# Kernel tuning notes

Hardware: AMD Instinct MI355X
Metric: run time of the kernel (lower is better)

Reference implementation:

```python
import jax, jax.numpy as jnp
import numpy as np

N = 100000   # nodes
E = 1600000  # edges
G = 512      # graphs
IN_F = 128
HID = 64
EPS = 1e-5


def setup_inputs() -> dict:
    key = jax.random.key(0)
    ks = jax.random.split(key, 16)
    x = jax.random.normal(ks[0], (N, IN_F), dtype=jnp.float32)
    edge_index = jax.random.randint(ks[1], (2, E), 0, N, dtype=jnp.int64)
    batch = jnp.sort(jax.random.randint(ks[2], (N,), 0, G, dtype=jnp.int64))
    s = 0.05
    return {
        'x': x, 'edge_index': edge_index, 'batch': batch,
        'W1': jax.random.normal(ks[3], (IN_F, HID), jnp.float32) * s,
        'b1': jax.random.normal(ks[4], (HID,), jnp.float32) * s,
        'g1': jax.random.uniform(ks[5], (HID,), jnp.float32),
        'be1': jax.random.normal(ks[6], (HID,), jnp.float32) * s,
        'rm1': jnp.zeros((HID,), jnp.float32),
        'rv1': jnp.ones((HID,), jnp.float32),
        'W2': jax.random.normal(ks[7], (HID, HID), jnp.float32) * s,
        'b2': jax.random.normal(ks[8], (HID,), jnp.float32) * s,
        'g2': jax.random.uniform(ks[9], (HID,), jnp.float32),
        'be2': jax.random.normal(ks[10], (HID,), jnp.float32) * s,
        'rm2': jnp.zeros((HID,), jnp.float32),
        'rv2': jnp.ones((HID,), jnp.float32),
        'Wh1': jax.random.normal(ks[11], (2 * HID, HID), jnp.float32) * s,
        'bh1': jax.random.normal(ks[12], (HID,), jnp.float32) * s,
        'Wh2': jax.random.normal(ks[13], (HID, HID // 2), jnp.float32) * s,
        'bh2': jnp.zeros((HID // 2,), jnp.float32),
        'Wh3': jax.random.normal(ks[14], (HID // 2, 1), jnp.float32) * s,
        'bh3': jnp.zeros((1,), jnp.float32),
    }


def _gcn(h, W, b, src, dst):
    # GCNConv with added self-loops and symmetric D^{-1/2} A D^{-1/2} normalization
    hw = h @ W                                   # [N, HID]
    deg = jnp.ones((N,), hw.dtype).at[dst].add(1.0)  # in-degree + self-loop
    dinv = jax.lax.rsqrt(deg)
    norm = dinv[src] * dinv[dst]                 # [E]
    agg = jax.ops.segment_sum(hw[src] * norm[:, None], dst, num_segments=N)
    return agg + hw * (dinv * dinv)[:, None] + b  # self-loop term + bias


def _bn(x, g, b, rm, rv):
    return (x - rm) * jax.lax.rsqrt(rv + EPS) * g + b


def reference(x, edge_index, batch, W1, b1, g1, be1, rm1, rv1,
              W2, b2, g2, be2, rm2, rv2, Wh1, bh1, Wh2, bh2, Wh3, bh3):
    src, dst = edge_index[0], edge_index[1]
    # layer 0 (no residual: dim change 128 -> 64)
    h = jax.nn.relu(_bn(_gcn(x, W1, b1, src, dst), g1, be1, rm1, rv1))
    # layer 1 with residual
    h = h + jax.nn.relu(_bn(_gcn(h, W2, b2, src, dst), g2, be2, rm2, rv2))
    # global mean + max pooling per graph
    ones = jnp.ones((N,), h.dtype)
    cnt = jnp.maximum(jax.ops.segment_sum(ones, batch, num_segments=G), 1.0)
    h_mean = jax.ops.segment_sum(h, batch, num_segments=G) / cnt[:, None]
    h_max = jax.ops.segment_max(h, batch, num_segments=G)
    hg = jnp.concatenate([h_mean, h_max], axis=-1)   # [G, 2*HID]
    # MLP head (dropout disabled in eval)
    z = jax.nn.relu(hg @ Wh1 + bh1)
    z = jax.nn.relu(z @ Wh2 + bh2)
    out = z @ Wh3 + bh3
    return jax.nn.sigmoid(out).squeeze(-1)           # [G]
```

## Files before the change

kernel.cpp:

```cpp
#include <hip/hip_runtime.h>
#include <math.h>

#define NN 100000
#define EE 1600000
#define GG 512
#define INF_ 128
#define HID 64
#define EPS 1e-5f

#define NBUK 391
#define P1_TILES 98
#define SETUP_B 25
#define POOL_WORDS (GG * 64 * 2 + GG)
#define ZERO_B ((POOL_WORDS + 255) / 256)

typedef unsigned int uint32;
typedef __attribute__((ext_vector_type(8))) short bf16x8;
typedef __attribute__((ext_vector_type(4))) float f32x4;

static __device__ inline uint32 f2bf(float f) {
    uint32 u = __float_as_uint(f);
    return (u + 0x7FFFu + ((u >> 16) & 1u)) >> 16;
}
static __device__ inline float bf_lo(uint32 u) { return __uint_as_float(u << 16); }
static __device__ inline float bf_hi(uint32 u) { return __uint_as_float(u & 0xFFFF0000u); }


__global__ __launch_bounds__(256) void k_hist1(const int* __restrict__ ei,
        int* __restrict__ hblk,
        const float* b1, const float* g1, const float* be1,
        const float* rm1, const float* rv1,
        const float* b2, const float* g2, const float* be2,
        const float* rm2, const float* rv2, float* sc,
        const float* W1, uint32* Wt1b, const float* W2, uint32* Wt2b,
        float* poolz) {
    int b = blockIdx.x, t = threadIdx.x;
    if (b < P1_TILES) {
        __shared__ int h[NBUK];
        for (int i = t; i < NBUK; i += 256) h[i] = 0;
        __syncthreads();
        const int4* dst4 = (const int4*)(ei + EE);
        int base4 = b * 4096;
        for (int j = 0; j < 16; ++j) {
            int i4 = base4 + j * 256 + t;
            if (i4 < EE / 4) {
                int4 d = dst4[i4];
                atomicAdd(&h[d.x >> 8], 1);
                atomicAdd(&h[d.y >> 8], 1);
                atomicAdd(&h[d.z >> 8], 1);
                atomicAdd(&h[d.w >> 8], 1);
            }
        }
        __syncthreads();
        for (int i = t; i < NBUK; i += 256) hblk[b * NBUK + i] = h[i];
    } else if (b < P1_TILES + SETUP_B) {
        int i = (b - P1_TILES) * 256 + t;
        if (i < 4096) {
            int n = i >> 6, kp = (i & 63) * 2;
            Wt1b[i] = f2bf(W1[(size_t)kp * 64 + n]) |
                      (f2bf(W1[(size_t)(kp + 1) * 64 + n]) << 16);
        } else if (i < 6144) {
            int j = i - 4096;
            int n = j >> 5, kp = (j & 31) * 2;
            Wt2b[j] = f2bf(W2[(size_t)kp * 64 + n]) |
                      (f2bf(W2[(size_t)(kp + 1) * 64 + n]) << 16);
        } else if (i < 6208) {
            int l = i - 6144;
            float s1 = g1[l] * rsqrtf(rv1[l] + EPS);
            sc[l]       = s1;
            sc[64 + l]  = (b1[l] - rm1[l]) * s1 + be1[l];
            float s2 = g2[l] * rsqrtf(rv2[l] + EPS);
            sc[128 + l] = s2;
            sc[192 + l] = (b2[l] - rm2[l]) * s2 + be2[l];
        }
    } else {
        int i = (b - P1_TILES - SETUP_B) * 256 + t;
        if (i < POOL_WORDS) poolz[i] = 0.f;
    }
}

__global__ void k_scan2(const int* __restrict__ hblk, int* __restrict__ bbase,
                        int* __restrict__ rbase, int* __restrict__ offs,
                        uint32* __restrict__ hwb) {
    __shared__ int wsum[8];
    int t = threadIdx.x;
    int lane = t & 63, w = t >> 6;
    if (t < 32) hwb[(size_t)NN * 32 + t] = 0u;
    int c = 0;
    if (t < NBUK)
        for (int b = 0; b < P1_TILES; ++b) c += hblk[b * NBUK + t];
    int v = c;
    for (int d = 1; d < 64; d <<= 1) { int n = __shfl_up(v, d); if (lane >= d) v += n; }
    if (lane == 63) wsum[w] = v;
    __syncthreads();
    int pre = 0;
    for (int q = 0; q < w; ++q) pre += wsum[q];
    int excl = pre + v - c;
    if (t <= NBUK) bbase[t] = excl;
    if (t == 0) offs[NN] = EE;
    if (t < NBUK) {
        int run = excl;
        for (int b = 0; b < P1_TILES; ++b) {
            rbase[b * NBUK + t] = run;
            run += hblk[b * NBUK + t];
        }
    }
}

__global__ __launch_bounds__(256) void k_p1b(const int* __restrict__ ei,
                                             const int* __restrict__ rbase,
                                             uint32* __restrict__ pairs) {
    __shared__ int h[NBUK];
    int b = blockIdx.x, t = threadIdx.x;
    for (int i = t; i < NBUK; i += 256) h[i] = rbase[b * NBUK + i];
    __syncthreads();
    const int4* src4 = (const int4*)ei;
    const int4* dst4 = (const int4*)(ei + EE);
    int base4 = b * 4096;
    for (int j = 0; j < 16; ++j) {
        int i4 = base4 + j * 256 + t;
        if (i4 < EE / 4) {
            int4 d = dst4[i4];
            int4 s = src4[i4];
            int p0 = atomicAdd(&h[d.x >> 8], 1);
            pairs[p0] = ((uint32)s.x << 8) | (uint32)(d.x & 255);
            int p1 = atomicAdd(&h[d.y >> 8], 1);
            pairs[p1] = ((uint32)s.y << 8) | (uint32)(d.y & 255);
            int p2 = atomicAdd(&h[d.z >> 8], 1);
            pairs[p2] = ((uint32)s.z << 8) | (uint32)(d.z & 255);
            int p3 = atomicAdd(&h[d.w >> 8], 1);
            pairs[p3] = ((uint32)s.w << 8) | (uint32)(d.w & 255);
        }
    }
}

__global__ __launch_bounds__(256) void k_p2(const uint32* __restrict__ pairs,
                                            const int* __restrict__ bbase,
                                            int* __restrict__ offs, float* __restrict__ dinv,
                                            int* __restrict__ col) {
    int b = blockIdx.x, t = threadIdx.x;
    int nbase = b << 8;
    int ebase = bbase[b], eend = bbase[b + 1];
    int m = eend - ebase;
    __shared__ int cnt[256];
    __shared__ int wsum[4];
    cnt[t] = 0;
    __syncthreads();
    for (int i = t; i < m; i += 256)
        atomicAdd(&cnt[pairs[ebase + i] & 255u], 1);
    __syncthreads();
    int c = cnt[t];
    int lane = t & 63, w = t >> 6;
    int v = c;
    for (int d = 1; d < 64; d <<= 1) { int n = __shfl_up(v, d); if (lane >= d) v += n; }
    if (lane == 63) wsum[w] = v;
    __syncthreads();
    int pre = 0;
    for (int q = 0; q < w; ++q) pre += wsum[q];
    int excl = pre + v - c;
    int node = nbase + t;
    if (node < NN) {
        offs[node] = ebase + excl;
        dinv[node] = rsqrtf(1.f + (float)c);
    }
    __syncthreads();
    cnt[t] = excl;
    __syncthreads();
    for (int i = t; i < m; i += 256) {
        uint32 u = pairs[ebase + i];
        int loc = atomicAdd(&cnt[u & 255u], 1);
        col[ebase + loc] = (int)(u >> 8);
    }
}

template <int K>
__global__ __launch_bounds__(256) void k_gemm_mfma(const float* __restrict__ X,
                                                   const uint32* __restrict__ Wtb,
                                                   const float* __restrict__ dinv,
                                                   uint32* __restrict__ outb, int nrows) {
    constexpr int KP = K + 8;
    __shared__ alignas(16) unsigned short Al[64 * KP];
    __shared__ alignas(16) unsigned short Bl[64 * KP];
    int tid = threadIdx.x;
    for (int i = tid; i < 64 * (K / 2); i += 256) {
        int n = i / (K / 2), kp = i % (K / 2);
        *(uint32*)&Bl[n * KP + kp * 2] = Wtb[i];
    }
    int r0 = blockIdx.x * 64;
    const float* Xb = X + (size_t)r0 * K;
    int limit = (nrows - r0) * K;
    for (int f = tid * 4; f < 64 * K; f += 1024) {
        float4 v = {0.f, 0.f, 0.f, 0.f};
        if (f + 3 < limit) v = *(const float4*)&Xb[f];
        int row = f / K, kpos = f % K;
        ushort4 pk;
        pk.x = (unsigned short)f2bf(v.x);
        pk.y = (unsigned short)f2bf(v.y);
        pk.z = (unsigned short)f2bf(v.z);
        pk.w = (unsigned short)f2bf(v.w);
        *(ushort4*)&Al[row * KP + kpos] = pk;
    }
    __syncthreads();
    int lane = tid & 63, wv = tid >> 6;
    int m = lane & 15, quad = lane >> 4;
    f32x4 acc0 = {0.f, 0.f, 0.f, 0.f}, acc1 = acc0, acc2 = acc0, acc3 = acc0;
    int arow = wv * 16 + m;
#pragma unroll
    for (int k0 = 0; k0 < K; k0 += 32) {
        int koff = k0 + quad * 8;
        bf16x8 a = *(const bf16x8*)&Al[arow * KP + koff];
        bf16x8 b0 = *(const bf16x8*)&Bl[(0 * 16 + m) * KP + koff];
        bf16x8 b1 = *(const bf16x8*)&Bl[(1 * 16 + m) * KP + koff];
        bf16x8 b2 = *(const bf16x8*)&Bl[(2 * 16 + m) * KP + koff];
        bf16x8 b3 = *(const bf16x8*)&Bl[(3 * 16 + m) * KP + koff];
        acc0 = __builtin_amdgcn_mfma_f32_16x16x32_bf16(a, b0, acc0, 0, 0, 0);
        acc1 = __builtin_amdgcn_mfma_f32_16x16x32_bf16(a, b1, acc1, 0, 0, 0);
        acc2 = __builtin_amdgcn_mfma_f32_16x16x32_bf16(a, b2, acc2, 0, 0, 0);
        acc3 = __builtin_amdgcn_mfma_f32_16x16x32_bf16(a, b3, acc3, 0, 0, 0);
    }
    float dv[4];
#pragma unroll
    for (int reg = 0; reg < 4; ++reg) {
        int row = r0 + wv * 16 + quad * 4 + reg;
        dv[reg] = (row < nrows) ? dinv[row] : 0.f;
    }
    const float* accs[4] = {(const float*)&acc0, (const float*)&acc1,
                            (const float*)&acc2, (const float*)&acc3};
#pragma unroll
    for (int nt = 0; nt < 4; ++nt) {
#pragma unroll
        for (int reg = 0; reg < 4; ++reg) {
            float val = accs[nt][reg] * dv[reg];
            float nxt = __shfl_down(val, 1);
            int row = r0 + wv * 16 + quad * 4 + reg;
            if (((m & 1) == 0) && row < nrows)
                outb[(size_t)row * 32 + nt * 8 + (m >> 1)] =
                    f2bf(val) | (f2bf(nxt) << 16);
        }
    }
}

__global__ void k_gcn_gather(const uint32* __restrict__ hwb, const int* __restrict__ col,
                             const int* __restrict__ offs,
                             const float* __restrict__ dinv, const float* __restrict__ scale,
                             const float* __restrict__ shift, const float* __restrict__ resid,
                             float* __restrict__ out) {
    int node = blockIdx.x * 4 + (threadIdx.x >> 6);
    if (node >= NN) return;
    int lane = threadIdx.x & 63;
    int half = lane >> 5;
    int fl = lane & 31;
    int e0 = offs[node], e1 = offs[node + 1];
    float di = dinv[node];
    uint32 uself = hwb[(size_t)node * 32 + fl];
    float ax0 = 0.f, ay0 = 0.f, ax1 = 0.f, ay1 = 0.f;
    for (int base = e0; base < e1; base += 64) {
        int m = e1 - base; if (m > 64) m = 64;
        int srcv = NN;
        if (lane < m) srcv = col[base + lane];
        for (int j = 0; j < m; j += 16) {
            int s0 = __shfl(srcv, j + half);
            int s1 = __shfl(srcv, j + 2 + half);
            int s2 = __shfl(srcv, j + 4 + half);
            int s3 = __shfl(srcv, j + 6 + half);
            int s4 = __shfl(srcv, j + 8 + half);
            int s5 = __shfl(srcv, j + 10 + half);
            int s6 = __shfl(srcv, j + 12 + half);
            int s7 = __shfl(srcv, j + 14 + half);
            uint32 u0 = hwb[(size_t)s0 * 32 + fl];
            uint32 u1 = hwb[(size_t)s1 * 32 + fl];
            uint32 u2 = hwb[(size_t)s2 * 32 + fl];
            uint32 u3 = hwb[(size_t)s3 * 32 + fl];
            uint32 u4 = hwb[(size_t)s4 * 32 + fl];
            uint32 u5 = hwb[(size_t)s5 * 32 + fl];
            uint32 u6 = hwb[(size_t)s6 * 32 + fl];
            uint32 u7 = hwb[(size_t)s7 * 32 + fl];
            ax0 += bf_lo(u0); ay0 += bf_hi(u0);
            ax1 += bf_lo(u1); ay1 += bf_hi(u1);
            ax0 += bf_lo(u2); ay0 += bf_hi(u2);
            ax1 += bf_lo(u3); ay1 += bf_hi(u3);
            ax0 += bf_lo(u4); ay0 += bf_hi(u4);
            ax1 += bf_lo(u5); ay1 += bf_hi(u5);
            ax0 += bf_lo(u6); ay0 += bf_hi(u6);
            ax1 += bf_lo(u7); ay1 += bf_hi(u7);
        }
    }
    float ax = ax0 + ax1, ay = ay0 + ay1;
    ax += __shfl(ax, fl + 32);
    ay += __shfl(ay, fl + 32);
    if (half == 0) {
        float vx = fmaf((ax + bf_lo(uself)) * di, scale[2 * fl],     shift[2 * fl]);
        float vy = fmaf((ay + bf_hi(uself)) * di, scale[2 * fl + 1], shift[2 * fl + 1]);
        vx = fmaxf(vx, 0.f);
        vy = fmaxf(vy, 0.f);
        if (resid) {
            float2 rv = *(const float2*)&resid[(size_t)node * 64 + 2 * fl];
            vx += rv.x; vy += rv.y;
        }
        float2 o; o.x = vx; o.y = vy;
        *(float2*)&out[(size_t)node * 64 + 2 * fl] = o;
    }
}

__global__ __launch_bounds__(256) void k_pool(const float* __restrict__ h,
                       const int* __restrict__ batch,
                       float* __restrict__ msum, float* __restrict__ mmax,
                       float* __restrict__ gcnt) {
    int lane = threadIdx.x & 63;
    int wv = threadIdx.x >> 6;
    int i0 = blockIdx.x * 128 + wv * 32;
    if (i0 >= NN) return;
    int i1 = i0 + 32; if (i1 > NN) i1 = NN;
    int cur = batch[i0];
    float sum = 0.f, mx = 0.f; int c = 0;
    for (int i = i0; i < i1; ++i) {
        int g = batch[i];
        if (g != cur) {
            atomicAdd(&msum[cur * 64 + lane], sum);
            atomicMax((unsigned int*)&mmax[cur * 64 + lane], __float_as_uint(mx));
            if (lane == 0) atomicAdd(&gcnt[cur], (float)c);
            sum = 0.f; mx = 0.f; c = 0; cur = g;
        }
        float v = h[(long)i * 64 + lane];
        sum += v; mx = fmaxf(mx, v); ++c;
    }
    atomicAdd(&msum[cur * 64 + lane], sum);
    atomicMax((unsigned int*)&mmax[cur * 64 + lane], __float_as_uint(mx));
    if (lane == 0) atomicAdd(&gcnt[cur], (float)c);
}

__global__ void k_head(const float* __restrict__ msum, const float* __restrict__ mmax,
                       const float* __restrict__ gcnt,
                       const float* __restrict__ Wh1, const float* __restrict__ bh1,
                       const float* __restrict__ Wh2, const float* __restrict__ bh2,
                       const float* __restrict__ Wh3, const float* __restrict__ bh3,
                       float* __restrict__ out) {
    int g = blockIdx.x, t = threadIdx.x;
    __shared__ float hg[128];
    __shared__ float z1[64];
    __shared__ float z2[32];
    float c = fmaxf(gcnt[g], 1.f);
    hg[t]      = msum[g * 64 + t] / c;
    hg[64 + t] = mmax[g * 64 + t];
    __syncthreads();
    float acc = bh1[t];
#pragma unroll 8
    for (int k = 0; k < 128; ++k) acc = fmaf(hg[k], Wh1[k * 64 + t], acc);
    z1[t] = fmaxf(acc, 0.f);
    __syncthreads();
    if (t < 32) {
        float a2 = bh2[t];
#pragma unroll 8
        for (int k = 0; k < 64; ++k) a2 = fmaf(z1[k], Wh2[k * 32 + t], a2);
        z2[t] = fmaxf(a2, 0.f);
    }
    __syncthreads();
    if (t == 0) {
        float a3 = bh3[0];
        for (int k = 0; k < 32; ++k) a3 = fmaf(z2[k], Wh3[k], a3);
        out[g] = 1.f / (1.f + expf(-a3));
    }
}


static inline size_t alignup(size_t x) { return (x + 255) & ~(size_t)255; }

extern "C" void kernel_launch(void* const* d_in, const int* in_sizes, int n_in,
                              void* d_out, int out_size, void* d_ws, size_t ws_size,
                              hipStream_t stream) {
    const float* x   = (const float*)d_in[0];
    const int*   ei  = (const int*)d_in[1];
    const int*   bat = (const int*)d_in[2];
    const float* W1  = (const float*)d_in[3];
    const float* b1  = (const float*)d_in[4];
    const float* g1  = (const float*)d_in[5];
    const float* be1 = (const float*)d_in[6];
    const float* rm1 = (const float*)d_in[7];
    const float* rv1 = (const float*)d_in[8];
    const float* W2  = (const float*)d_in[9];
    const float* b2  = (const float*)d_in[10];
    const float* g2  = (const float*)d_in[11];
    const float* be2 = (const float*)d_in[12];
    const float* rm2 = (const float*)d_in[13];
    const float* rv2 = (const float*)d_in[14];
    const float* Wh1 = (const float*)d_in[15];
    const float* bh1 = (const float*)d_in[16];
    const float* Wh2 = (const float*)d_in[17];
    const float* bh2 = (const float*)d_in[18];
    const float* Wh3 = (const float*)d_in[19];
    const float* bh3 = (const float*)d_in[20];
    float* out = (float*)d_out;

    char* ws = (char*)d_ws;
    size_t o = 0;
    int*   hblk   = (int*)(ws + o);  o = alignup(o + (size_t)P1_TILES * NBUK * 4);
    int*   rbase  = (int*)(ws + o);  o = alignup(o + (size_t)P1_TILES * NBUK * 4);
    int*   bbase  = (int*)(ws + o);  o = alignup(o + (NBUK + 1) * 4);
    int*   offs   = (int*)(ws + o);  o = alignup(o + (NN + 1) * 4);
    uint32* pairs = (uint32*)(ws + o); o = alignup(o + (size_t)EE * 4);
    int*   col    = (int*)(ws + o);  o = alignup(o + (size_t)EE * 4);
    float* dinv   = (float*)(ws + o); o = alignup(o + (size_t)NN * 4);
    float* scb    = (float*)(ws + o); o = alignup(o + 4 * 64 * 4);
    uint32* Wt1b  = (uint32*)(ws + o); o = alignup(o + 64 * (INF_ / 2) * 4);
    uint32* Wt2b  = (uint32*)(ws + o); o = alignup(o + 64 * (HID / 2) * 4);
    float* msum   = (float*)(ws + o); o += (size_t)GG * 64 * 4;
    float* mmax   = (float*)(ws + o); o += (size_t)GG * 64 * 4;
    float* gcnt   = (float*)(ws + o); o += (size_t)GG * 4;
    o = alignup(o);
    uint32* hwb   = (uint32*)(ws + o); o = alignup(o + (size_t)(NN + 1) * 32 * 4);
    float* h      = (float*)(ws + o); o = alignup(o + (size_t)NN * 64 * 4);
    (void)ws_size; (void)n_in; (void)in_sizes; (void)out_size;

    k_hist1<<<P1_TILES + SETUP_B + ZERO_B, 256, 0, stream>>>(
        ei, hblk, b1, g1, be1, rm1, rv1, b2, g2, be2, rm2, rv2, scb,
        W1, Wt1b, W2, Wt2b, msum);
    k_scan2<<<1, 512, 0, stream>>>(hblk, bbase, rbase, offs, hwb);
    k_p1b<<<P1_TILES, 256, 0, stream>>>(ei, rbase, pairs);
    k_p2<<<NBUK, 256, 0, stream>>>(pairs, bbase, offs, dinv, col);

    k_gemm_mfma<INF_><<<(NN + 63) / 64, 256, 0, stream>>>(x, Wt1b, dinv, hwb, NN);
    k_gcn_gather<<<(NN + 3) / 4, 256, 0, stream>>>(hwb, col, offs, dinv,
                                                   scb, scb + 64, nullptr, h);
    k_gemm_mfma<HID><<<(NN + 63) / 64, 256, 0, stream>>>(h, Wt2b, dinv, hwb, NN);
    k_gcn_gather<<<(NN + 3) / 4, 256, 0, stream>>>(hwb, col, offs, dinv,
                                                   scb + 128, scb + 192, h, h);
    k_pool<<<(NN + 127) / 128, 256, 0, stream>>>(h, bat, msum, mmax, gcnt);
    k_head<<<GG, 64, 0, stream>>>(msum, mmax, gcnt, Wh1, bh1, Wh2, bh2, Wh3, bh3, out);
}
```

Measured before the change: 305.8 us.

## Fuse layer-1 GEMM into setup kernel and merge pooling into MLP head

Layer 1 now computes X@W1 without the dinv scale, so its GEMM can run in the first kernel alongside the edge histogram and graph-boundary computation. The layer-1 gather applies dinv per edge instead, reading it for each source. Weight transposes to bf16 move into the GEMM bodies, and BN folding moves into the scan kernel. Pooling uses precomputed per-graph node ranges inside the head kernel, removing atomics and the zeroing pass, at the cost of extra per-edge dinv loads and serial per-graph reduction.

```diff
diff --git a/kernel.cpp b/kernel.cpp
--- a/kernel.cpp
+++ b/kernel.cpp
@@ -10,9 +10,8 @@
 
 #define NBUK 391
 #define P1_TILES 98
-#define SETUP_B 25
-#define POOL_WORDS (GG * 64 * 2 + GG)
-#define ZERO_B ((POOL_WORDS + 255) / 256)
+#define GB_B 25
+#define GEMM1_B 1563
 
 typedef unsigned int uint32;
 typedef __attribute__((ext_vector_type(8))) short bf16x8;
@@ -26,17 +25,82 @@
 static __device__ inline float bf_hi(uint32 u) { return __uint_as_float(u & 0xFFFF0000u); }
 
 
-__global__ __launch_bounds__(256) void k_hist1(const int* __restrict__ ei,
-        int* __restrict__ hblk,
-        const float* b1, const float* g1, const float* be1,
-        const float* rm1, const float* rv1,
-        const float* b2, const float* g2, const float* be2,
-        const float* rm2, const float* rv2, float* sc,
-        const float* W1, uint32* Wt1b, const float* W2, uint32* Wt2b,
-        float* poolz) {
+template <int K, bool SCALE>
+__device__ __forceinline__ void gemm_body(const float* __restrict__ X,
+        const float* __restrict__ W, const float* __restrict__ dinv,
+        uint32* __restrict__ outb, int nrows, int bx,
+        unsigned short* __restrict__ Al, unsigned short* __restrict__ Bl) {
+    constexpr int KP = K + 8;
+    int tid = threadIdx.x;
+    for (int i = tid; i < 64 * (K / 2); i += 256) {
+        int n = i & 63, kp = i >> 6;
+        uint32 lo = f2bf(W[(size_t)(2 * kp) * 64 + n]);
+        uint32 hi = f2bf(W[(size_t)(2 * kp + 1) * 64 + n]);
+        *(uint32*)&Bl[n * KP + kp * 2] = lo | (hi << 16);
+    }
+    int r0 = bx * 64;
+    const float* Xb = X + (size_t)r0 * K;
+    int limit = (nrows - r0) * K;
+    for (int f = tid * 4; f < 64 * K; f += 1024) {
+        float4 v = {0.f, 0.f, 0.f, 0.f};
+        if (f + 3 < limit) v = *(const float4*)&Xb[f];
+        int row = f / K, kpos = f % K;
+        ushort4 pk;
+        pk.x = (unsigned short)f2bf(v.x);
+        pk.y = (unsigned short)f2bf(v.y);
+        pk.z = (unsigned short)f2bf(v.z);
+        pk.w = (unsigned short)f2bf(v.w);
+        *(ushort4*)&Al[row * KP + kpos] = pk;
+    }
+    __syncthreads();
+    int lane = tid & 63, wv = tid >> 6;
+    int m = lane & 15, quad = lane >> 4;
+    f32x4 acc0 = {0.f, 0.f, 0.f, 0.f}, acc1 = acc0, acc2 = acc0, acc3 = acc0;
+    int arow = wv * 16 + m;
+#pragma unroll
+    for (int k0 = 0; k0 < K; k0 += 32) {
+        int koff = k0 + quad * 8;
+        bf16x8 a = *(const bf16x8*)&Al[arow * KP + koff];
+        bf16x8 b0 = *(const bf16x8*)&Bl[(0 * 16 + m) * KP + koff];
+        bf16x8 b1 = *(const bf16x8*)&Bl[(1 * 16 + m) * KP + koff];
+        bf16x8 b2 = *(const bf16x8*)&Bl[(2 * 16 + m) * KP + koff];
+        bf16x8 b3 = *(const bf16x8*)&Bl[(3 * 16 + m) * KP + koff];
+        acc0 = __builtin_amdgcn_mfma_f32_16x16x32_bf16(a, b0, acc0, 0, 0, 0);
+        acc1 = __builtin_amdgcn_mfma_f32_16x16x32_bf16(a, b1, acc1, 0, 0, 0);
+        acc2 = __builtin_amdgcn_mfma_f32_16x16x32_bf16(a, b2, acc2, 0, 0, 0);
+        acc3 = __builtin_amdgcn_mfma_f32_16x16x32_bf16(a, b3, acc3, 0, 0, 0);
+    }
+    float dv[4];
+#pragma unroll
+    for (int reg = 0; reg < 4; ++reg) {
+        int row = r0 + wv * 16 + quad * 4 + reg;
+        if (SCALE) dv[reg] = (row < nrows) ? dinv[row] : 0.f;
+        else       dv[reg] = 1.f;
+    }
+    const float* accs[4] = {(const float*)&acc0, (const float*)&acc1,
+                            (const float*)&acc2, (const float*)&acc3};
+#pragma unroll
+    for (int nt = 0; nt < 4; ++nt) {
+#pragma unroll
+        for (int reg = 0; reg < 4; ++reg) {
+            float val = accs[nt][reg] * dv[reg];
+            float nxt = __shfl_down(val, 1);
+            int row = r0 + wv * 16 + quad * 4 + reg;
+            if (((m & 1) == 0) && row < nrows)
+                outb[(size_t)row * 32 + nt * 8 + (m >> 1)] =
+                    f2bf(val) | (f2bf(nxt) << 16);
+        }
+    }
+}
+
+__global__ __launch_bounds__(256) void k_mega(const int* __restrict__ ei,
+        int* __restrict__ hblk, const int* __restrict__ bat, int* __restrict__ gb,
+        const float* __restrict__ x, const float* __restrict__ W1,
+        uint32* __restrict__ hwb) {
+    __shared__ alignas(16) char smem[64 * (INF_ + 8) * 2 * 2];
     int b = blockIdx.x, t = threadIdx.x;
     if (b < P1_TILES) {
-        __shared__ int h[NBUK];
+        int* h = (int*)smem;
         for (int i = t; i < NBUK; i += 256) h[i] = 0;
         __syncthreads();
         const int4* dst4 = (const int4*)(ei + EE);
@@ -53,39 +117,47 @@
         }
         __syncthreads();
         for (int i = t; i < NBUK; i += 256) hblk[b * NBUK + i] = h[i];
-    } else if (b < P1_TILES + SETUP_B) {
-        int i = (b - P1_TILES) * 256 + t;
-        if (i < 4096) {
-            int n = i >> 6, kp = (i & 63) * 2;
-            Wt1b[i] = f2bf(W1[(size_t)kp * 64 + n]) |
-                      (f2bf(W1[(size_t)(kp + 1) * 64 + n]) << 16);
-        } else if (i < 6144) {
-            int j = i - 4096;
-            int n = j >> 5, kp = (j & 31) * 2;
-            Wt2b[j] = f2bf(W2[(size_t)kp * 64 + n]) |
-                      (f2bf(W2[(size_t)(kp + 1) * 64 + n]) << 16);
-        } else if (i < 6208) {
-            int l = i - 6144;
-            float s1 = g1[l] * rsqrtf(rv1[l] + EPS);
-            sc[l]       = s1;
-            sc[64 + l]  = (b1[l] - rm1[l]) * s1 + be1[l];
-            float s2 = g2[l] * rsqrtf(rv2[l] + EPS);
-            sc[128 + l] = s2;
-            sc[192 + l] = (b2[l] - rm2[l]) * s2 + be2[l];
+    } else if (b < P1_TILES + GB_B) {
+        int gid = (b - P1_TILES) * 256 + t;
+        for (int i = gid; i < NN; i += GB_B * 256) {
+            int bi = bat[i];
+            if (i == 0) {
+                for (int g = 0; g <= bi; ++g) gb[g] = 0;
+            } else {
+                int bp = bat[i - 1];
+                for (int g = bp + 1; g <= bi; ++g) gb[g] = i;
+            }
+            if (i == NN - 1)
+                for (int g = bi + 1; g <= GG; ++g) gb[g] = NN;
         }
     } else {
-        int i = (b - P1_TILES - SETUP_B) * 256 + t;
-        if (i < POOL_WORDS) poolz[i] = 0.f;
+        int bx = b - P1_TILES - GB_B;
+        unsigned short* Al = (unsigned short*)smem;
+        unsigned short* Bl = (unsigned short*)(smem + 64 * (INF_ + 8) * 2);
+        gemm_body<INF_, false>(x, W1, nullptr, hwb, NN, bx, Al, Bl);
     }
 }
 
 __global__ void k_scan2(const int* __restrict__ hblk, int* __restrict__ bbase,
                         int* __restrict__ rbase, int* __restrict__ offs,
-                        uint32* __restrict__ hwb) {
+                        uint32* __restrict__ hwb,
+                        const float* b1, const float* g1, const float* be1,
+                        const float* rm1, const float* rv1,
+                        const float* b2, const float* g2, const float* be2,
+                        const float* rm2, const float* rv2, float* sc) {
     __shared__ int wsum[8];
     int t = threadIdx.x;
     int lane = t & 63, w = t >> 6;
     if (t < 32) hwb[(size_t)NN * 32 + t] = 0u;
+    if (t >= 448) {
+        int l = t - 448;
+        float s1 = g1[l] * rsqrtf(rv1[l] + EPS);
+        sc[l]       = s1;
+        sc[64 + l]  = (b1[l] - rm1[l]) * s1 + be1[l];
+        float s2 = g2[l] * rsqrtf(rv2[l] + EPS);
+        sc[128 + l] = s2;
+        sc[192 + l] = (b2[l] - rm2[l]) * s2 + be2[l];
+    }
     int c = 0;
     if (t < NBUK)
         for (int b = 0; b < P1_TILES; ++b) c += hblk[b * NBUK + t];
@@ -173,70 +245,70 @@
     }
 }
 
-template <int K>
-__global__ __launch_bounds__(256) void k_gemm_mfma(const float* __restrict__ X,
-                                                   const uint32* __restrict__ Wtb,
-                                                   const float* __restrict__ dinv,
-                                                   uint32* __restrict__ outb, int nrows) {
-    constexpr int KP = K + 8;
-    __shared__ alignas(16) unsigned short Al[64 * KP];
-    __shared__ alignas(16) unsigned short Bl[64 * KP];
-    int tid = threadIdx.x;
-    for (int i = tid; i < 64 * (K / 2); i += 256) {
-        int n = i / (K / 2), kp = i % (K / 2);
-        *(uint32*)&Bl[n * KP + kp * 2] = Wtb[i];
-    }
-    int r0 = blockIdx.x * 64;
-    const float* Xb = X + (size_t)r0 * K;
-    int limit = (nrows - r0) * K;
-    for (int f = tid * 4; f < 64 * K; f += 1024) {
-        float4 v = {0.f, 0.f, 0.f, 0.f};
-        if (f + 3 < limit) v = *(const float4*)&Xb[f];
-        int row = f / K, kpos = f % K;
-        ushort4 pk;
-        pk.x = (unsigned short)f2bf(v.x);
-        pk.y = (unsigned short)f2bf(v.y);
-        pk.z = (unsigned short)f2bf(v.z);
-        pk.w = (unsigned short)f2bf(v.w);
-        *(ushort4*)&Al[row * KP + kpos] = pk;
-    }
-    __syncthreads();
-    int lane = tid & 63, wv = tid >> 6;
-    int m = lane & 15, quad = lane >> 4;
-    f32x4 acc0 = {0.f, 0.f, 0.f, 0.f}, acc1 = acc0, acc2 = acc0, acc3 = acc0;
-    int arow = wv * 16 + m;
-#pragma unroll
-    for (int k0 = 0; k0 < K; k0 += 32) {
-        int koff = k0 + quad * 8;
-        bf16x8 a = *(const bf16x8*)&Al[arow * KP + koff];
-        bf16x8 b0 = *(const bf16x8*)&Bl[(0 * 16 + m) * KP + koff];
-        bf16x8 b1 = *(const bf16x8*)&Bl[(1 * 16 + m) * KP + koff];
-        bf16x8 b2 = *(const bf16x8*)&Bl[(2 * 16 + m) * KP + koff];
-        bf16x8 b3 = *(const bf16x8*)&Bl[(3 * 16 + m) * KP + koff];
-        acc0 = __builtin_amdgcn_mfma_f32_16x16x32_bf16(a, b0, acc0, 0, 0, 0);
-        acc1 = __builtin_amdgcn_mfma_f32_16x16x32_bf16(a, b1, acc1, 0, 0, 0);
-        acc2 = __builtin_amdgcn_mfma_f32_16x16x32_bf16(a, b2, acc2, 0, 0, 0);
-        acc3 = __builtin_amdgcn_mfma_f32_16x16x32_bf16(a, b3, acc3, 0, 0, 0);
-    }
-    float dv[4];
-#pragma unroll
-    for (int reg = 0; reg < 4; ++reg) {
-        int row = r0 + wv * 16 + quad * 4 + reg;
-        dv[reg] = (row < nrows) ? dinv[row] : 0.f;
-    }
-    const float* accs[4] = {(const float*)&acc0, (const float*)&acc1,
-                            (const float*)&acc2, (const float*)&acc3};
-#pragma unroll
-    for (int nt = 0; nt < 4; ++nt) {
-#pragma unroll
-        for (int reg = 0; reg < 4; ++reg) {
-            float val = accs[nt][reg] * dv[reg];
-            float nxt = __shfl_down(val, 1);
-            int row = r0 + wv * 16 + quad * 4 + reg;
-            if (((m & 1) == 0) && row < nrows)
-                outb[(size_t)row * 32 + nt * 8 + (m >> 1)] =
-                    f2bf(val) | (f2bf(nxt) << 16);
-        }
+__global__ void k_gcn_gather_w(const uint32* __restrict__ hwb, const int* __restrict__ col,
+                               const int* __restrict__ offs,
+                               const float* __restrict__ dinv, const float* __restrict__ scale,
+                               const float* __restrict__ shift,
+                               float* __restrict__ out) {
+    int node = blockIdx.x * 4 + (threadIdx.x >> 6);
+    if (node >= NN) return;
+    int lane = threadIdx.x & 63;
+    int half = lane >> 5;
+    int fl = lane & 31;
+    int e0 = offs[node], e1 = offs[node + 1];
+    float di = dinv[node];
+    uint32 uself = hwb[(size_t)node * 32 + fl];
+    float ax0 = 0.f, ay0 = 0.f, ax1 = 0.f, ay1 = 0.f;
+    for (int base = e0; base < e1; base += 64) {
+        int m = e1 - base; if (m > 64) m = 64;
+        int srcv = NN; float wv = 0.f;
+        if (lane < m) { srcv = col[base + lane]; wv = dinv[srcv]; }
+        for (int j = 0; j < m; j += 16) {
+            int   s0 = __shfl(srcv, j + half);
+            int   s1 = __shfl(srcv, j + 2 + half);
+            int   s2 = __shfl(srcv, j + 4 + half);
+            int   s3 = __shfl(srcv, j + 6 + half);
+            int   s4 = __shfl(srcv, j + 8 + half);
+            int   s5 = __shfl(srcv, j + 10 + half);
+            int   s6 = __shfl(srcv, j + 12 + half);
+            int   s7 = __shfl(srcv, j + 14 + half);
+            float w0 = __shfl(wv, j + half);
+            float w1 = __shfl(wv, j + 2 + half);
+            float w2 = __shfl(wv, j + 4 + half);
+            float w3 = __shfl(wv, j + 6 + half);
+            float w4 = __shfl(wv, j + 8 + half);
+            float w5 = __shfl(wv, j + 10 + half);
+            float w6 = __shfl(wv, j + 12 + half);
+            float w7 = __shfl(wv, j + 14 + half);
+            uint32 u0 = hwb[(size_t)s0 * 32 + fl];
+            uint32 u1 = hwb[(size_t)s1 * 32 + fl];
+            uint32 u2 = hwb[(size_t)s2 * 32 + fl];
+            uint32 u3 = hwb[(size_t)s3 * 32 + fl];
+            uint32 u4 = hwb[(size_t)s4 * 32 + fl];
+            uint32 u5 = hwb[(size_t)s5 * 32 + fl];
+            uint32 u6 = hwb[(size_t)s6 * 32 + fl];
+            uint32 u7 = hwb[(size_t)s7 * 32 + fl];
+            ax0 = fmaf(bf_lo(u0), w0, ax0); ay0 = fmaf(bf_hi(u0), w0, ay0);
+            ax1 = fmaf(bf_lo(u1), w1, ax1); ay1 = fmaf(bf_hi(u1), w1, ay1);
+            ax0 = fmaf(bf_lo(u2), w2, ax0); ay0 = fmaf(bf_hi(u2), w2, ay0);
+            ax1 = fmaf(bf_lo(u3), w3, ax1); ay1 = fmaf(bf_hi(u3), w3, ay1);
+            ax0 = fmaf(bf_lo(u4), w4, ax0); ay0 = fmaf(bf_hi(u4), w4, ay0);
+            ax1 = fmaf(bf_lo(u5), w5, ax1); ay1 = fmaf(bf_hi(u5), w5, ay1);
+            ax0 = fmaf(bf_lo(u6), w6, ax0); ay0 = fmaf(bf_hi(u6), w6, ay0);
+            ax1 = fmaf(bf_lo(u7), w7, ax1); ay1 = fmaf(bf_hi(u7), w7, ay1);
+        }
+    }
+    float ax = ax0 + ax1, ay = ay0 + ay1;
+    ax += __shfl(ax, fl + 32);
+    ay += __shfl(ay, fl + 32);
+    if (half == 0) {
+        float dii = di * di;
+        float vx = fmaf(ax * di + bf_lo(uself) * dii, scale[2 * fl],     shift[2 * fl]);
+        float vy = fmaf(ay * di + bf_hi(uself) * dii, scale[2 * fl + 1], shift[2 * fl + 1]);
+        vx = fmaxf(vx, 0.f);
+        vy = fmaxf(vy, 0.f);
+        float2 o; o.x = vx; o.y = vy;
+        *(float2*)&out[(size_t)node * 64 + 2 * fl] = o;
     }
 }
 
@@ -302,46 +374,49 @@
     }
 }
 
-__global__ __launch_bounds__(256) void k_pool(const float* __restrict__ h,
-                       const int* __restrict__ batch,
-                       float* __restrict__ msum, float* __restrict__ mmax,
-                       float* __restrict__ gcnt) {
-    int lane = threadIdx.x & 63;
-    int wv = threadIdx.x >> 6;
-    int i0 = blockIdx.x * 128 + wv * 32;
-    if (i0 >= NN) return;
-    int i1 = i0 + 32; if (i1 > NN) i1 = NN;
-    int cur = batch[i0];
-    float sum = 0.f, mx = 0.f; int c = 0;
-    for (int i = i0; i < i1; ++i) {
-        int g = batch[i];
-        if (g != cur) {
-            atomicAdd(&msum[cur * 64 + lane], sum);
-            atomicMax((unsigned int*)&mmax[cur * 64 + lane], __float_as_uint(mx));
-            if (lane == 0) atomicAdd(&gcnt[cur], (float)c);
-            sum = 0.f; mx = 0.f; c = 0; cur = g;
-        }
-        float v = h[(long)i * 64 + lane];
-        sum += v; mx = fmaxf(mx, v); ++c;
-    }
-    atomicAdd(&msum[cur * 64 + lane], sum);
-    atomicMax((unsigned int*)&mmax[cur * 64 + lane], __float_as_uint(mx));
-    if (lane == 0) atomicAdd(&gcnt[cur], (float)c);
-}
-
-__global__ void k_head(const float* __restrict__ msum, const float* __restrict__ mmax,
-                       const float* __restrict__ gcnt,
-                       const float* __restrict__ Wh1, const float* __restrict__ bh1,
-                       const float* __restrict__ Wh2, const float* __restrict__ bh2,
-                       const float* __restrict__ Wh3, const float* __restrict__ bh3,
-                       float* __restrict__ out) {
+__global__ void k_poolhead(const float* __restrict__ h, const int* __restrict__ gb,
+                           const float* __restrict__ Wh1, const float* __restrict__ bh1,
+                           const float* __restrict__ Wh2, const float* __restrict__ bh2,
+                           const float* __restrict__ Wh3, const float* __restrict__ bh3,
+                           float* __restrict__ out) {
     int g = blockIdx.x, t = threadIdx.x;
+    int lo = gb[g], hi = gb[g + 1];
+    float s0 = 0.f, s1 = 0.f, s2 = 0.f, s3 = 0.f;
+    float s4 = 0.f, s5 = 0.f, s6 = 0.f, s7 = 0.f;
+    float m0 = 0.f, m1 = 0.f, m2 = 0.f, m3 = 0.f;
+    float m4 = 0.f, m5 = 0.f, m6 = 0.f, m7 = 0.f;
+    int i = lo;
+    for (; i + 8 <= hi; i += 8) {
+        float v0 = h[(size_t)(i + 0) * 64 + t];
+        float v1 = h[(size_t)(i + 1) * 64 + t];
+        float v2 = h[(size_t)(i + 2) * 64 + t];
+        float v3 = h[(size_t)(i + 3) * 64 + t];
+        float v4 = h[(size_t)(i + 4) * 64 + t];
+        float v5 = h[(size_t)(i + 5) * 64 + t];
+        float v6 = h[(size_t)(i + 6) * 64 + t];
+        float v7 = h[(size_t)(i + 7) * 64 + t];
+        s0 += v0; m0 = fmaxf(m0, v0);
+        s1 += v1; m1 = fmaxf(m1, v1);
+        s2 += v2; m2 = fmaxf(m2, v2);
+        s3 += v3; m3 = fmaxf(m3, v3);
+        s4 += v4; m4 = fmaxf(m4, v4);
+        s5 += v5; m5 = fmaxf(m5, v5);
+        s6 += v6; m6 = fmaxf(m6, v6);
+        s7 += v7; m7 = fmaxf(m7, v7);
+    }
+    for (; i < hi; ++i) {
+        float v = h[(size_t)i * 64 + t];
+        s0 += v; m0 = fmaxf(m0, v);
+    }
+    float sum = ((s0 + s1) + (s2 + s3)) + ((s4 + s5) + (s6 + s7));
+    float mx = fmaxf(fmaxf(fmaxf(m0, m1), fmaxf(m2, m3)),
+                     fmaxf(fmaxf(m4, m5), fmaxf(m6, m7)));
+    float c = fmaxf((float)(hi - lo), 1.f);
     __shared__ float hg[128];
     __shared__ float z1[64];
     __shared__ float z2[32];
-    float c = fmaxf(gcnt[g], 1.f);
-    hg[t]      = msum[g * 64 + t] / c;
-    hg[64 + t] = mmax[g * 64 + t];
+    hg[t]      = sum / c;
+    hg[64 + t] = mx;
     __syncthreads();
     float acc = bh1[t];
 #pragma unroll 8
@@ -360,6 +435,15 @@
         for (int k = 0; k < 32; ++k) a3 = fmaf(z2[k], Wh3[k], a3);
         out[g] = 1.f / (1.f + expf(-a3));
     }
+}
+
+__global__ __launch_bounds__(256) void k_gemm2(const float* __restrict__ X,
+                                               const float* __restrict__ W,
+                                               const float* __restrict__ dinv,
+                                               uint32* __restrict__ outb) {
+    __shared__ alignas(16) unsigned short Al[64 * (HID + 8)];
+    __shared__ alignas(16) unsigned short Bl[64 * (HID + 8)];
+    gemm_body<HID, true>(X, W, dinv, outb, NN, blockIdx.x, Al, Bl);
 }
 
 
@@ -401,29 +485,22 @@
     int*   col    = (int*)(ws + o);  o = alignup(o + (size_t)EE * 4);
     float* dinv   = (float*)(ws + o); o = alignup(o + (size_t)NN * 4);
     float* scb    = (float*)(ws + o); o = alignup(o + 4 * 64 * 4);
-    uint32* Wt1b  = (uint32*)(ws + o); o = alignup(o + 64 * (INF_ / 2) * 4);
-    uint32* Wt2b  = (uint32*)(ws + o); o = alignup(o + 64 * (HID / 2) * 4);
-    float* msum   = (float*)(ws + o); o += (size_t)GG * 64 * 4;
-    float* mmax   = (float*)(ws + o); o += (size_t)GG * 64 * 4;
-    float* gcnt   = (float*)(ws + o); o += (size_t)GG * 4;
-    o = alignup(o);
+    int*   gb     = (int*)(ws + o);  o = alignup(o + (GG + 1) * 4);
     uint32* hwb   = (uint32*)(ws + o); o = alignup(o + (size_t)(NN + 1) * 32 * 4);
     float* h      = (float*)(ws + o); o = alignup(o + (size_t)NN * 64 * 4);
     (void)ws_size; (void)n_in; (void)in_sizes; (void)out_size;
 
-    k_hist1<<<P1_TILES + SETUP_B + ZERO_B, 256, 0, stream>>>(
-        ei, hblk, b1, g1, be1, rm1, rv1, b2, g2, be2, rm2, rv2, scb,
-        W1, Wt1b, W2, Wt2b, msum);
-    k_scan2<<<1, 512, 0, stream>>>(hblk, bbase, rbase, offs, hwb);
+    k_mega<<<P1_TILES + GB_B + GEMM1_B, 256, 0, stream>>>(ei, hblk, bat, gb,
+                                                          x, W1, hwb);
+    k_scan2<<<1, 512, 0, stream>>>(hblk, bbase, rbase, offs, hwb,
+                                   b1, g1, be1, rm1, rv1, b2, g2, be2, rm2, rv2, scb);
     k_p1b<<<P1_TILES, 256, 0, stream>>>(ei, rbase, pairs);
     k_p2<<<NBUK, 256, 0, stream>>>(pairs, bbase, offs, dinv, col);
 
-    k_gemm_mfma<INF_><<<(NN + 63) / 64, 256, 0, stream>>>(x, Wt1b, dinv, hwb, NN);
-    k_gcn_gather<<<(NN + 3) / 4, 256, 0, stream>>>(hwb, col, offs, dinv,
-                                                   scb, scb + 64, nullptr, h);
-    k_gemm_mfma<HID><<<(NN + 63) / 64, 256, 0, stream>>>(h, Wt2b, dinv, hwb, NN);
+    k_gcn_gather_w<<<(NN + 3) / 4, 256, 0, stream>>>(hwb, col, offs, dinv,
+                                                     scb, scb + 64, h);
+    k_gemm2<<<GEMM1_B, 256, 0, stream>>>(h, W2, dinv, hwb);
     k_gcn_gather<<<(NN + 3) / 4, 256, 0, stream>>>(hwb, col, offs, dinv,
                                                    scb + 128, scb + 192, h, h);
-    k_pool<<<(NN + 127) / 128, 256, 0, stream>>>(h, bat, msum, mmax, gcnt);
-    k_head<<<GG, 64, 0, stream>>>(msum, mmax, gcnt, Wh1, bh1, Wh2, bh2, Wh3, bh3, out);
-}
+    k_poolhead<<<GG, 64, 0, stream>>>(h, gb, Wh1, bh1, Wh2, bh2, Wh3, bh3, out);
+}
```

After: 297.7 us. 1.03x faster.
